# Kernel tuning notes

Measured on AMD Instinct MI355X. Metric: run time of the kernel, lower is better.

## Reference

```python
import jax, jax.numpy as jnp
import numpy as np

DT = 0.2
DX = 0.0327249  # 2*pi/192
KPAD = 2  # (kernel_size-1)//2 for 5x5 periodic 'same' padding
# total derivative order of fd00, fd01, fd10, fd02, fd11, fd20
_ORD = np.array([0, 1, 1, 2, 2, 2], dtype=np.float32)
_SCALES = (DX ** -_ORD)  # FD2d scale = dx^-(jx+jy)


def _poly_apply(w0, b0, w1, b1, wf, bf, x):
    # SymNet (expr.poly): each hidden layer computes two linear combos and
    # appends their product as a new channel; final linear -> scalar.
    o = x @ w0.T + b0                                        # [..., 2]
    x = jnp.concatenate([x, o[..., :1] * o[..., 1:2]], -1)   # [..., 13]
    o = x @ w1.T + b1
    x = jnp.concatenate([x, o[..., :1] * o[..., 1:2]], -1)   # [..., 14]
    return (x @ wf.T + bf)[..., 0]


def _rhs(u, kernels, pw0, pb0, pw1, pb1, pwf, pbf):
    # u: [B, C, H, W]
    B, C, H, W = u.shape
    ks = kernels * jnp.asarray(_SCALES, u.dtype)[:, None, None]   # [6,5,5]
    k01f = -ks[1, :, ::-1]   # -flip along width  (torch flip([3]))
    k10f = -ks[2, ::-1, :]   # -flip along height (torch flip([2]))
    kall = jnp.concatenate([ks, k01f[None], k10f[None]], 0)[:, None]  # [8,1,5,5]
    up = jnp.pad(u, ((0, 0), (0, 0), (KPAD, KPAD), (KPAD, KPAD)), mode='wrap')
    up = up.reshape(B * C, 1, H + 2 * KPAD, W + 2 * KPAD)
    D = jax.lax.conv_general_dilated(up, kall, (1, 1), 'VALID')   # [B*C,8,H,W]
    D = D.reshape(B, C, 8, H, W)
    # per-channel blocks ordered (00,01,10,02,11,20)
    base = jnp.transpose(D[:, :, :6], (0, 3, 4, 1, 2)).reshape(B, H, W, C * 6)
    f01 = jnp.transpose(D[:, :, 6], (0, 2, 3, 1))   # [B,H,W,C]
    f10 = jnp.transpose(D[:, :, 7], (0, 2, 3, 1))
    # upwind: pick normal vs flipped 1st-order stencil by sign of d(poly_k)/d(u01/u10)
    Xsel = base
    for k in range(C):
        pk = (pw0[k], pb0[k], pw1[k], pb1[k], pwf[k], pbf[k])
        G = jax.grad(lambda z: _poly_apply(*pk, z).sum())(base)   # [B,H,W,C*6]
        g01, g10 = G[..., k * 6 + 1], G[..., k * 6 + 2]
        u01 = jnp.where(g01 > 0, base[..., k * 6 + 1], f01[..., k])
        u10 = jnp.where(g10 > 0, base[..., k * 6 + 2], f10[..., k])
        Xsel = Xsel.at[..., k * 6 + 1].set(u01).at[..., k * 6 + 2].set(u10)
    uadd = jnp.stack(
        [_poly_apply(pw0[k], pb0[k], pw1[k], pb1[k], pwf[k], pbf[k], Xsel)
         for k in range(C)], axis=1)                              # [B,C,H,W]
    return uadd


def setup_inputs() -> dict:
    key = jax.random.key(0)
    ks = jax.random.split(key, 8)
    f32 = jnp.float32
    inp = {
        'init': jax.random.normal(ks[0], (16, 2, 192, 192), f32),
        'kernels': jax.random.normal(ks[1], (6, 5, 5), f32) * 0.002,
        'poly_w0': jax.random.normal(ks[2], (2, 2, 12), f32) * 0.01,
        'poly_b0': jax.random.normal(ks[3], (2, 2), f32) * 0.01,
        'poly_w1': jax.random.normal(ks[4], (2, 2, 13), f32) * 0.01,
        'poly_b1': jax.random.normal(ks[5], (2, 2), f32) * 0.01,
        'poly_wf': jax.random.normal(ks[6], (2, 1, 14), f32) * 0.01,
        'poly_bf': jax.random.normal(ks[7], (2, 1), f32) * 0.01,
        'T': 1,
    }
    return inp


def reference(init, kernels, poly_w0, poly_b0, poly_w1, poly_b1, poly_wf, poly_bf, T):
    stepnum = int(round(T / DT))  # 5 RK2 (midpoint) steps
    u = init
    for _ in range(stepnum):
        uh = u + (DT / 2) * _rhs(u, kernels, poly_w0, poly_b0, poly_w1, poly_b1, poly_wf, poly_bf)
        u = u + DT * _rhs(uh, kernels, poly_w0, poly_b0, poly_w1, poly_b1, poly_wf, poly_bf)
    return u
```

## Files before the change

### kernel.cpp

```cpp
#include <hip/hip_runtime.h>

typedef float v2f __attribute__((ext_vector_type(2)));

#define HH 192
#define WW 192
#define BATCH 16
#define PLANE (HH*WW)
#define NELEM (BATCH*2*PLANE)

#define TILEX 96
#define TILEY 8
#define SW 100
#define SH2 12
#define NSITE (SH2*SW)

__global__ void prep_kernel(const float* __restrict__ kern,
                            const float* __restrict__ pw0, const float* __restrict__ pb0,
                            const float* __restrict__ pw1, const float* __restrict__ pb1,
                            const float* __restrict__ pwf, const float* __restrict__ pbf,
                            float* __restrict__ ws)
{
    int t = blockIdx.x * blockDim.x + threadIdx.x;
    if (t < 200) {
        const float inv  = 1.0f / 0.0327249f;
        const float inv2 = inv * inv;
        const float sc[6] = {1.0f, inv, inv, inv2, inv2, inv2};
        int o = t / 8, j = t % 8, dy = o / 5, dx = o % 5;
        float v;
        if (j < 6)       v =  kern[j*25 + dy*5 + dx] * sc[j];
        else if (j == 6) v = -kern[1*25 + dy*5 + (4-dx)] * sc[1];
        else             v = -kern[2*25 + (4-dy)*5 + dx] * sc[2];
        ws[o*8 + j] = v;
    } else if (t < 279) {
        int p = t - 200;
        int arr, a, b;
        if (p < 12)       { arr=0; a=p;      b=24+p; }
        else if (p < 24)  { int i=p-12; arr=0; a=12+i; b=36+i; }
        else if (p == 24) { arr=1; a=0; b=2; }
        else if (p == 25) { arr=1; a=1; b=3; }
        else if (p < 38)  { int i=p-26; arr=2; a=i;    b=26+i; }
        else if (p < 50)  { int i=p-38; arr=2; a=13+i; b=39+i; }
        else if (p == 50) { arr=2; a=12; b=38; }
        else if (p == 51) { arr=2; a=25; b=51; }
        else if (p == 52) { arr=3; a=0; b=2; }
        else if (p == 53) { arr=3; a=1; b=3; }
        else if (p < 68)  { int i=p-54; arr=4; a=i; b=14+i; }
        else if (p == 68) { arr=5; a=0; b=1; }
        else {
            const signed char   A0[10] = {1,2,13,14,1,2,14,15,1,2};
            const signed char   A1[10] = {31,32,43,44,33,34,46,47,21,22};
            const unsigned char AR[10] = {0,0,0,0,2,2,2,2,4,4};
            int i = p - 69; arr = AR[i]; a = A0[i]; b = A1[i];
        }
        const float* bases[6] = {pw0, pb0, pw1, pb1, pwf, pbf};
        v2f v; v[0] = bases[arr][a]; v[1] = bases[arr][b];
        ((v2f*)(ws + 256))[p] = v;
    }
}

__global__ __launch_bounds__(256, 3) void rhs_kernel(
    const float* __restrict__ uin,
    const float* __restrict__ ubase,
    float* __restrict__ uout,
    const float* __restrict__ ws,
    float alpha)
{
    const float* K8T = ws;
    const v2f* PP = (const v2f*)(ws + 256);

    __shared__ v2f sh[SH2][SW];
    const int b   = blockIdx.z;
    const int ty0 = blockIdx.y * TILEY;
    const int tx0 = blockIdx.x * TILEX;
    const int tid = threadIdx.x;
    const size_t bo = (size_t)b * 2 * PLANE;

    const float* uin_b = uin + bo;
    for (int i = tid; i < NSITE; i += 256) {
        const int ly  = i / SW;
        const int col = i - ly * SW;
        int gy = ty0 + ly - 2;  if (gy < 0) gy += HH; else if (gy >= HH) gy -= HH;
        int gx = tx0 + col - 2; if (gx < 0) gx += WW; else if (gx >= WW) gx -= WW;
        const int gi = gy*WW + gx;
        v2f v; v[0] = uin_b[gi]; v[1] = uin_b[PLANE + gi];
        sh[ly][col] = v;
    }
    __syncthreads();

    const int cy = tid >> 5;
    const int x3 = (tid & 31) * 3;

    v2f D2[3][8];
    #pragma unroll
    for (int p = 0; p < 3; ++p)
        #pragma unroll
        for (int j = 0; j < 8; ++j)
            D2[p][j] = (v2f){0.0f, 0.0f};

    #pragma unroll 1
    for (int dy = 0; dy < 5; ++dy) {
        v2f row[7];
        #pragma unroll
        for (int dx = 0; dx < 7; ++dx)
            row[dx] = sh[cy + dy][x3 + dx];
        const float* Kt = K8T + dy * 40;
        #pragma unroll
        for (int dx = 0; dx < 5; ++dx) {
            #pragma unroll
            for (int j = 0; j < 8; ++j) {
                const float w = Kt[dx*8 + j];
                D2[0][j] += row[dx]   * w;
                D2[1][j] += row[dx+1] * w;
                D2[2][j] += row[dx+2] * w;
            }
        }
    }

#define Z(p,i) (D2[p][(i)%6][(i)/6])

    v2f res[3];
    #pragma unroll
    for (int p = 0; p < 3; ++p) {
        v2f o0 = PP[24], o1 = PP[25];
        #pragma unroll
        for (int i = 0; i < 12; ++i) {
            const float zv = Z(p, i);
            o0 += PP[i]    * zv;
            o1 += PP[12+i] * zv;
        }
        const v2f pb = o0 * o1;
        v2f q0 = PP[52] + PP[50]*pb;
        v2f q1 = PP[53] + PP[51]*pb;
        #pragma unroll
        for (int i = 0; i < 12; ++i) {
            const float zv = Z(p, i);
            q0 += PP[26+i] * zv;
            q1 += PP[38+i] * zv;
        }

        const v2f t1 = o1*PP[69] + o0*PP[71];
        const v2f g1 = PP[77] + PP[66]*t1
            + PP[67]*(q1*(PP[73] + PP[50]*t1) + q0*(PP[75] + PP[51]*t1));
        const v2f t2 = o1*PP[70] + o0*PP[72];
        const v2f g2 = PP[78] + PP[66]*t2
            + PP[67]*(q1*(PP[74] + PP[50]*t2) + q0*(PP[76] + PP[51]*t2));

        const float s1 = (g1[0] > 0.0f) ? Z(p,1) : D2[p][6][0];
        const float s2 = (g2[0] > 0.0f) ? Z(p,2) : D2[p][7][0];
        const float s3 = (g1[1] > 0.0f) ? Z(p,7) : D2[p][6][1];
        const float s4 = (g2[1] > 0.0f) ? Z(p,8) : D2[p][7][1];
#define XV(i) ((i)==1 ? s1 : (i)==2 ? s2 : (i)==7 ? s3 : (i)==8 ? s4 : Z(p,(i)))

        v2f f0 = PP[24], f1 = PP[25];
        #pragma unroll
        for (int i = 0; i < 12; ++i) {
            const float xv = XV(i);
            f0 += PP[i]    * xv;
            f1 += PP[12+i] * xv;
        }
        const v2f pf = f0 * f1;
        v2f r0 = PP[52] + PP[50]*pf;
        v2f r1 = PP[53] + PP[51]*pf;
        v2f y  = PP[68] + PP[66]*pf;
        #pragma unroll
        for (int i = 0; i < 12; ++i) {
            const float xv = XV(i);
            r0 += PP[26+i] * xv;
            r1 += PP[38+i] * xv;
            y  += PP[54+i] * xv;
        }
        res[p] = y + PP[67]*(r0*r1);
#undef XV
    }

    const int oy = ty0 + cy, ox = tx0 + x3;
    const size_t o0i = bo + (size_t)oy * WW + ox;
    #pragma unroll
    for (int p = 0; p < 3; ++p) {
        uout[o0i + p]         = ubase[o0i + p]         + alpha * res[p][0];
        uout[o0i + PLANE + p] = ubase[o0i + PLANE + p] + alpha * res[p][1];
    }
}

extern "C" void kernel_launch(void* const* d_in, const int* in_sizes, int n_in,
                              void* d_out, int out_size, void* d_ws, size_t ws_size,
                              hipStream_t stream)
{
    const float* init = (const float*)d_in[0];
    const float* kern = (const float*)d_in[1];
    const float* pw0  = (const float*)d_in[2];
    const float* pb0  = (const float*)d_in[3];
    const float* pw1  = (const float*)d_in[4];
    const float* pb1  = (const float*)d_in[5];
    const float* pwf  = (const float*)d_in[6];
    const float* pbf  = (const float*)d_in[7];
    float* out = (float*)d_out;
    float* ws  = (float*)d_ws;

    float* bufA = ws + 512;
    float* bufH = bufA + NELEM;

    prep_kernel<<<dim3(1), dim3(320), 0, stream>>>(kern, pw0, pb0, pw1, pb1, pwf, pbf, ws);

    const dim3 grid(WW/TILEX, HH/TILEY, BATCH);
    const dim3 block(256);
    const float DTF = 0.2f, DTH = 0.1f;

    rhs_kernel<<<grid, block, 0, stream>>>(init, init, bufH, ws, DTH);
    rhs_kernel<<<grid, block, 0, stream>>>(bufH, init, bufA, ws, DTF);
    for (int s = 0; s < 3; ++s) {
        rhs_kernel<<<grid, block, 0, stream>>>(bufA, bufA, bufH, ws, DTH);
        rhs_kernel<<<grid, block, 0, stream>>>(bufH, bufA, bufA, ws, DTF);
    }
    rhs_kernel<<<grid, block, 0, stream>>>(bufA, bufA, bufH, ws, DTH);
    rhs_kernel<<<grid, block, 0, stream>>>(bufH, bufA, out,  ws, DTF);
}
```

Baseline: 201.3 us.

## Fuse all RK2 stages into one persistent kernel with neighbor-tile flag sync

```diff
diff --git a/kernel.cpp b/kernel.cpp
--- a/kernel.cpp
+++ b/kernel.cpp
@@ -13,6 +13,13 @@
 #define SW 100
 #define SH2 12
 #define NSITE (SH2*SW)
+#define NTILES 768
+#define DTF 0.2f
+#define DTH 0.1f
+
+#define WS_PP    256
+#define WS_FLAGS 512
+#define WS_BUF   8192
 
 __global__ void prep_kernel(const float* __restrict__ kern,
                             const float* __restrict__ pw0, const float* __restrict__ pb0,
@@ -54,131 +61,199 @@
         }
         const float* bases[6] = {pw0, pb0, pw1, pb1, pwf, pbf};
         v2f v; v[0] = bases[arr][a]; v[1] = bases[arr][b];
-        ((v2f*)(ws + 256))[p] = v;
+        ((v2f*)(ws + WS_PP))[p] = v;
     }
+    unsigned* flags = (unsigned*)(ws + WS_FLAGS);
+    for (int i = t; i < 9 * NTILES; i += 320) flags[i] = 0u;
 }
 
-__global__ __launch_bounds__(256, 3) void rhs_kernel(
-    const float* __restrict__ uin,
-    const float* __restrict__ ubase,
-    float* __restrict__ uout,
-    const float* __restrict__ ws,
-    float alpha)
+union DV { double d; v2f v; };
+
+__global__ __launch_bounds__(256, 3) void mega_kernel(
+    const float* __restrict__ init,
+    float* __restrict__ out,
+    float* __restrict__ ws)
 {
     const float* K8T = ws;
-    const v2f* PP = (const v2f*)(ws + 256);
+    const v2f* PP = (const v2f*)(ws + WS_PP);
+    unsigned* flags = (unsigned*)(ws + WS_FLAGS);
+    v2f* P0 = (v2f*)(ws + WS_BUF);
+    v2f* P1 = P0 + (NELEM / 2);
 
     __shared__ v2f sh[SH2][SW];
     const int b   = blockIdx.z;
-    const int ty0 = blockIdx.y * TILEY;
-    const int tx0 = blockIdx.x * TILEX;
+    const int bx  = blockIdx.x;
+    const int by  = blockIdx.y;
+    const int ty0 = by * TILEY;
+    const int tx0 = bx * TILEX;
     const int tid = threadIdx.x;
-    const size_t bo = (size_t)b * 2 * PLANE;
-
-    const float* uin_b = uin + bo;
-    for (int i = tid; i < NSITE; i += 256) {
-        const int ly  = i / SW;
-        const int col = i - ly * SW;
-        int gy = ty0 + ly - 2;  if (gy < 0) gy += HH; else if (gy >= HH) gy -= HH;
-        int gx = tx0 + col - 2; if (gx < 0) gx += WW; else if (gx >= WW) gx -= WW;
-        const int gi = gy*WW + gx;
-        v2f v; v[0] = uin_b[gi]; v[1] = uin_b[PLANE + gi];
-        sh[ly][col] = v;
-    }
-    __syncthreads();
+    const int myflat = b * 48 + by * 2 + bx;
 
     const int cy = tid >> 5;
     const int x3 = (tid & 31) * 3;
-
-    v2f D2[3][8];
-    #pragma unroll
-    for (int p = 0; p < 3; ++p)
+    const int oy = ty0 + cy, ox = tx0 + x3;
+    const size_t site0 = (size_t)b * PLANE + (size_t)oy * WW + ox;
+
+    float base0[3], base1[3];
+
+    #pragma unroll 1
+    for (int s = 0; s < 10; ++s) {
+        const float alpha = (s & 1) ? DTF : DTH;
+        const v2f* Pr = (s & 1) ? P0 : P1;
+        v2f*       Pw = (s & 1) ? P1 : P0;
+
+        if (s) {
+            if (tid < 6) {
+                int ny = by + (tid >> 1) - 1;
+                if (ny < 0) ny += 24; else if (ny >= 24) ny -= 24;
+                const int nc = (tid & 1) ? (1 - bx) : bx;
+                const unsigned* f = flags + (s - 1) * NTILES + (b * 48 + ny * 2 + nc);
+                while (!__hip_atomic_load(f, __ATOMIC_RELAXED, __HIP_MEMORY_SCOPE_AGENT))
+                    __builtin_amdgcn_s_sleep(1);
+            }
+            __syncthreads();
+        }
+
+        if (s == 0) {
+            const float* init_b = init + (size_t)b * 2 * PLANE;
+            for (int i = tid; i < NSITE; i += 256) {
+                const int ly  = i / SW;
+                const int col = i - ly * SW;
+                int gy = ty0 + ly - 2;  if (gy < 0) gy += HH; else if (gy >= HH) gy -= HH;
+                int gx = tx0 + col - 2; if (gx < 0) gx += WW; else if (gx >= WW) gx -= WW;
+                const int gi = gy*WW + gx;
+                v2f v; v[0] = init_b[gi]; v[1] = init_b[PLANE + gi];
+                sh[ly][col] = v;
+            }
+        } else {
+            const v2f* Pb = Pr + (size_t)b * PLANE;
+            for (int i = tid; i < NSITE; i += 256) {
+                const int ly  = i / SW;
+                const int col = i - ly * SW;
+                int gy = ty0 + ly - 2;  if (gy < 0) gy += HH; else if (gy >= HH) gy -= HH;
+                int gx = tx0 + col - 2; if (gx < 0) gx += WW; else if (gx >= WW) gx -= WW;
+                DV cv;
+                cv.d = __hip_atomic_load((const double*)(Pb + gy*WW + gx),
+                                         __ATOMIC_RELAXED, __HIP_MEMORY_SCOPE_AGENT);
+                sh[ly][col] = cv.v;
+            }
+        }
+        __syncthreads();
+
+        if (s == 0) {
+            #pragma unroll
+            for (int p = 0; p < 3; ++p) {
+                const v2f v = sh[cy+2][x3+2+p];
+                base0[p] = v[0]; base1[p] = v[1];
+            }
+        }
+
+        v2f D2[3][8];
         #pragma unroll
-        for (int j = 0; j < 8; ++j)
-            D2[p][j] = (v2f){0.0f, 0.0f};
-
-    #pragma unroll 1
-    for (int dy = 0; dy < 5; ++dy) {
-        v2f row[7];
+        for (int p = 0; p < 3; ++p)
+            #pragma unroll
+            for (int j = 0; j < 8; ++j)
+                D2[p][j] = (v2f){0.0f, 0.0f};
+
+        #pragma unroll 1
+        for (int dy = 0; dy < 5; ++dy) {
+            v2f row[7];
+            #pragma unroll
+            for (int dx = 0; dx < 7; ++dx)
+                row[dx] = sh[cy + dy][x3 + dx];
+            const float* Kt = K8T + dy * 40;
+            #pragma unroll
+            for (int dx = 0; dx < 5; ++dx) {
+                #pragma unroll
+                for (int j = 0; j < 8; ++j) {
+                    const float w = Kt[dx*8 + j];
+                    D2[0][j] += row[dx]   * w;
+                    D2[1][j] += row[dx+1] * w;
+                    D2[2][j] += row[dx+2] * w;
+                }
+            }
+        }
+
+#define Z(p,i) (D2[p][(i)%6][(i)/6])
+
+        v2f res[3];
         #pragma unroll
-        for (int dx = 0; dx < 7; ++dx)
-            row[dx] = sh[cy + dy][x3 + dx];
-        const float* Kt = K8T + dy * 40;
-        #pragma unroll
-        for (int dx = 0; dx < 5; ++dx) {
-            #pragma unroll
-            for (int j = 0; j < 8; ++j) {
-                const float w = Kt[dx*8 + j];
-                D2[0][j] += row[dx]   * w;
-                D2[1][j] += row[dx+1] * w;
-                D2[2][j] += row[dx+2] * w;
-            }
-        }
-    }
-
-#define Z(p,i) (D2[p][(i)%6][(i)/6])
-
-    v2f res[3];
-    #pragma unroll
-    for (int p = 0; p < 3; ++p) {
-        v2f o0 = PP[24], o1 = PP[25];
-        #pragma unroll
-        for (int i = 0; i < 12; ++i) {
-            const float zv = Z(p, i);
-            o0 += PP[i]    * zv;
-            o1 += PP[12+i] * zv;
-        }
-        const v2f pb = o0 * o1;
-        v2f q0 = PP[52] + PP[50]*pb;
-        v2f q1 = PP[53] + PP[51]*pb;
-        #pragma unroll
-        for (int i = 0; i < 12; ++i) {
-            const float zv = Z(p, i);
-            q0 += PP[26+i] * zv;
-            q1 += PP[38+i] * zv;
-        }
-
-        const v2f t1 = o1*PP[69] + o0*PP[71];
-        const v2f g1 = PP[77] + PP[66]*t1
-            + PP[67]*(q1*(PP[73] + PP[50]*t1) + q0*(PP[75] + PP[51]*t1));
-        const v2f t2 = o1*PP[70] + o0*PP[72];
-        const v2f g2 = PP[78] + PP[66]*t2
-            + PP[67]*(q1*(PP[74] + PP[50]*t2) + q0*(PP[76] + PP[51]*t2));
-
-        const float s1 = (g1[0] > 0.0f) ? Z(p,1) : D2[p][6][0];
-        const float s2 = (g2[0] > 0.0f) ? Z(p,2) : D2[p][7][0];
-        const float s3 = (g1[1] > 0.0f) ? Z(p,7) : D2[p][6][1];
-        const float s4 = (g2[1] > 0.0f) ? Z(p,8) : D2[p][7][1];
+        for (int p = 0; p < 3; ++p) {
+            v2f o0 = PP[24], o1 = PP[25];
+            #pragma unroll
+            for (int i = 0; i < 12; ++i) {
+                const float zv = Z(p, i);
+                o0 += PP[i]    * zv;
+                o1 += PP[12+i] * zv;
+            }
+            const v2f pb = o0 * o1;
+            v2f q0 = PP[52] + PP[50]*pb;
+            v2f q1 = PP[53] + PP[51]*pb;
+            #pragma unroll
+            for (int i = 0; i < 12; ++i) {
+                const float zv = Z(p, i);
+                q0 += PP[26+i] * zv;
+                q1 += PP[38+i] * zv;
+            }
+
+            const v2f t1 = o1*PP[69] + o0*PP[71];
+            const v2f g1 = PP[77] + PP[66]*t1
+                + PP[67]*(q1*(PP[73] + PP[50]*t1) + q0*(PP[75] + PP[51]*t1));
+            const v2f t2 = o1*PP[70] + o0*PP[72];
+            const v2f g2 = PP[78] + PP[66]*t2
+                + PP[67]*(q1*(PP[74] + PP[50]*t2) + q0*(PP[76] + PP[51]*t2));
+
+            const float s1 = (g1[0] > 0.0f) ? Z(p,1) : D2[p][6][0];
+            const float s2 = (g2[0] > 0.0f) ? Z(p,2) : D2[p][7][0];
+            const float s3 = (g1[1] > 0.0f) ? Z(p,7) : D2[p][6][1];
+            const float s4 = (g2[1] > 0.0f) ? Z(p,8) : D2[p][7][1];
 #define XV(i) ((i)==1 ? s1 : (i)==2 ? s2 : (i)==7 ? s3 : (i)==8 ? s4 : Z(p,(i)))
 
-        v2f f0 = PP[24], f1 = PP[25];
-        #pragma unroll
-        for (int i = 0; i < 12; ++i) {
-            const float xv = XV(i);
-            f0 += PP[i]    * xv;
-            f1 += PP[12+i] * xv;
-        }
-        const v2f pf = f0 * f1;
-        v2f r0 = PP[52] + PP[50]*pf;
-        v2f r1 = PP[53] + PP[51]*pf;
-        v2f y  = PP[68] + PP[66]*pf;
-        #pragma unroll
-        for (int i = 0; i < 12; ++i) {
-            const float xv = XV(i);
-            r0 += PP[26+i] * xv;
-            r1 += PP[38+i] * xv;
-            y  += PP[54+i] * xv;
-        }
-        res[p] = y + PP[67]*(r0*r1);
+            v2f f0 = PP[24], f1 = PP[25];
+            #pragma unroll
+            for (int i = 0; i < 12; ++i) {
+                const float xv = XV(i);
+                f0 += PP[i]    * xv;
+                f1 += PP[12+i] * xv;
+            }
+            const v2f pf = f0 * f1;
+            v2f r0 = PP[52] + PP[50]*pf;
+            v2f r1 = PP[53] + PP[51]*pf;
+            v2f y  = PP[68] + PP[66]*pf;
+            #pragma unroll
+            for (int i = 0; i < 12; ++i) {
+                const float xv = XV(i);
+                r0 += PP[26+i] * xv;
+                r1 += PP[38+i] * xv;
+                y  += PP[54+i] * xv;
+            }
+            res[p] = y + PP[67]*(r0*r1);
 #undef XV
-    }
-
-    const int oy = ty0 + cy, ox = tx0 + x3;
-    const size_t o0i = bo + (size_t)oy * WW + ox;
-    #pragma unroll
-    for (int p = 0; p < 3; ++p) {
-        uout[o0i + p]         = ubase[o0i + p]         + alpha * res[p][0];
-        uout[o0i + PLANE + p] = ubase[o0i + PLANE + p] + alpha * res[p][1];
+        }
+
+        if (s == 9) {
+            const size_t o0i = (size_t)b * 2 * PLANE + (size_t)oy * WW + ox;
+            #pragma unroll
+            for (int p = 0; p < 3; ++p) {
+                out[o0i + p]         = base0[p] + alpha * res[p][0];
+                out[o0i + PLANE + p] = base1[p] + alpha * res[p][1];
+            }
+        } else {
+            v2f* dst = Pw + site0;
+            #pragma unroll
+            for (int p = 0; p < 3; ++p) {
+                const float w0v = base0[p] + alpha * res[p][0];
+                const float w1v = base1[p] + alpha * res[p][1];
+                DV cv; cv.v = (v2f){w0v, w1v};
+                __hip_atomic_store((double*)(dst + p), cv.d,
+                                   __ATOMIC_RELAXED, __HIP_MEMORY_SCOPE_AGENT);
+                if (s & 1) { base0[p] = w0v; base1[p] = w1v; }
+            }
+            __syncthreads();
+            if (tid == 0)
+                __hip_atomic_store(flags + s * NTILES + myflat, 1u,
+                                   __ATOMIC_RELAXED, __HIP_MEMORY_SCOPE_AGENT);
+        }
     }
 }
 
@@ -197,21 +272,8 @@
     float* out = (float*)d_out;
     float* ws  = (float*)d_ws;
 
-    float* bufA = ws + 512;
-    float* bufH = bufA + NELEM;
-
     prep_kernel<<<dim3(1), dim3(320), 0, stream>>>(kern, pw0, pb0, pw1, pb1, pwf, pbf, ws);
 
     const dim3 grid(WW/TILEX, HH/TILEY, BATCH);
-    const dim3 block(256);
-    const float DTF = 0.2f, DTH = 0.1f;
-
-    rhs_kernel<<<grid, block, 0, stream>>>(init, init, bufH, ws, DTH);
-    rhs_kernel<<<grid, block, 0, stream>>>(bufH, init, bufA, ws, DTF);
-    for (int s = 0; s < 3; ++s) {
-        rhs_kernel<<<grid, block, 0, stream>>>(bufA, bufA, bufH, ws, DTH);
-        rhs_kernel<<<grid, block, 0, stream>>>(bufH, bufA, bufA, ws, DTF);
-    }
-    rhs_kernel<<<grid, block, 0, stream>>>(bufA, bufA, bufH, ws, DTH);
-    rhs_kernel<<<grid, block, 0, stream>>>(bufH, bufA, out,  ws, DTF);
+    mega_kernel<<<grid, dim3(256), 0, stream>>>(init, out, ws);
 }
```

New measurement: 488.8 us. +142.9%, slower.

## Fuse both RK2 midpoint stages into one kernel with halo recomputation

Applied to the files above, without the earlier changes.

```diff
diff --git a/kernel.cpp b/kernel.cpp
--- a/kernel.cpp
+++ b/kernel.cpp
@@ -10,9 +10,14 @@
 
 #define TILEX 96
 #define TILEY 8
-#define SW 100
-#define SH2 12
-#define NSITE (SH2*SW)
+#define SWW 104
+#define SHH 16
+#define UHW 100
+#define UHH 12
+#define NSU (SHH*SWW)
+#define NSH (UHH*UHW)
+#define DTF 0.2f
+#define DTH 0.1f
 
 __global__ void prep_kernel(const float* __restrict__ kern,
                             const float* __restrict__ pw0, const float* __restrict__ pb0,
@@ -58,17 +63,71 @@
     }
 }
 
-__global__ __launch_bounds__(256, 3) void rhs_kernel(
+__device__ __forceinline__ v2f poly_site(const v2f* __restrict__ PP, const v2f D2[8])
+{
+#define Z1(i) (D2[(i)%6][(i)/6])
+    v2f o0 = PP[24], o1 = PP[25];
+    #pragma unroll
+    for (int i = 0; i < 12; ++i) {
+        const float zv = Z1(i);
+        o0 += PP[i]    * zv;
+        o1 += PP[12+i] * zv;
+    }
+    const v2f pb = o0 * o1;
+    v2f q0 = PP[52] + PP[50]*pb;
+    v2f q1 = PP[53] + PP[51]*pb;
+    #pragma unroll
+    for (int i = 0; i < 12; ++i) {
+        const float zv = Z1(i);
+        q0 += PP[26+i] * zv;
+        q1 += PP[38+i] * zv;
+    }
+    const v2f t1 = o1*PP[69] + o0*PP[71];
+    const v2f g1 = PP[77] + PP[66]*t1
+        + PP[67]*(q1*(PP[73] + PP[50]*t1) + q0*(PP[75] + PP[51]*t1));
+    const v2f t2 = o1*PP[70] + o0*PP[72];
+    const v2f g2 = PP[78] + PP[66]*t2
+        + PP[67]*(q1*(PP[74] + PP[50]*t2) + q0*(PP[76] + PP[51]*t2));
+
+    const float s1 = (g1[0] > 0.0f) ? Z1(1) : D2[6][0];
+    const float s2 = (g2[0] > 0.0f) ? Z1(2) : D2[7][0];
+    const float s3 = (g1[1] > 0.0f) ? Z1(7) : D2[6][1];
+    const float s4 = (g2[1] > 0.0f) ? Z1(8) : D2[7][1];
+#define XV1(i) ((i)==1 ? s1 : (i)==2 ? s2 : (i)==7 ? s3 : (i)==8 ? s4 : Z1(i))
+
+    v2f f0 = PP[24], f1 = PP[25];
+    #pragma unroll
+    for (int i = 0; i < 12; ++i) {
+        const float xv = XV1(i);
+        f0 += PP[i]    * xv;
+        f1 += PP[12+i] * xv;
+    }
+    const v2f pf = f0 * f1;
+    v2f r0 = PP[52] + PP[50]*pf;
+    v2f r1 = PP[53] + PP[51]*pf;
+    v2f y  = PP[68] + PP[66]*pf;
+    #pragma unroll
+    for (int i = 0; i < 12; ++i) {
+        const float xv = XV1(i);
+        r0 += PP[26+i] * xv;
+        r1 += PP[38+i] * xv;
+        y  += PP[54+i] * xv;
+    }
+    return y + PP[67]*(r0*r1);
+#undef XV1
+#undef Z1
+}
+
+__global__ __launch_bounds__(256, 3) void step_kernel(
     const float* __restrict__ uin,
-    const float* __restrict__ ubase,
     float* __restrict__ uout,
-    const float* __restrict__ ws,
-    float alpha)
+    const float* __restrict__ ws)
 {
     const float* K8T = ws;
     const v2f* PP = (const v2f*)(ws + 256);
 
-    __shared__ v2f sh[SH2][SW];
+    __shared__ v2f shU[SHH][SWW];
+    __shared__ v2f shH[UHH][UHW];
     const int b   = blockIdx.z;
     const int ty0 = blockIdx.y * TILEY;
     const int tx0 = blockIdx.x * TILEX;
@@ -76,109 +135,86 @@
     const size_t bo = (size_t)b * 2 * PLANE;
 
     const float* uin_b = uin + bo;
-    for (int i = tid; i < NSITE; i += 256) {
-        const int ly  = i / SW;
-        const int col = i - ly * SW;
-        int gy = ty0 + ly - 2;  if (gy < 0) gy += HH; else if (gy >= HH) gy -= HH;
-        int gx = tx0 + col - 2; if (gx < 0) gx += WW; else if (gx >= WW) gx -= WW;
+    for (int i = tid; i < NSU; i += 256) {
+        const int ly  = i / SWW;
+        const int col = i - ly * SWW;
+        int gy = ty0 + ly - 4;  if (gy < 0) gy += HH; else if (gy >= HH) gy -= HH;
+        int gx = tx0 + col - 4; if (gx < 0) gx += WW; else if (gx >= WW) gx -= WW;
         const int gi = gy*WW + gx;
         v2f v; v[0] = uin_b[gi]; v[1] = uin_b[PLANE + gi];
-        sh[ly][col] = v;
+        shU[ly][col] = v;
+    }
+    __syncthreads();
+
+    #pragma unroll 1
+    for (int i = tid; i < NSH; i += 256) {
+        const int ly  = i / UHW;
+        const int col = i - ly * UHW;
+
+        v2f D2[8];
+        #pragma unroll
+        for (int j = 0; j < 8; ++j) D2[j] = (v2f){0.0f, 0.0f};
+
+        #pragma unroll 1
+        for (int dy = 0; dy < 5; ++dy) {
+            v2f w0 = shU[ly+dy][col  ];
+            v2f w1 = shU[ly+dy][col+1];
+            v2f w2 = shU[ly+dy][col+2];
+            v2f w3 = shU[ly+dy][col+3];
+            v2f w4 = shU[ly+dy][col+4];
+            const float* Kt = K8T + dy * 40;
+            #pragma unroll
+            for (int j = 0; j < 8; ++j) {
+                D2[j] += w0 * Kt[j];
+                D2[j] += w1 * Kt[8+j];
+                D2[j] += w2 * Kt[16+j];
+                D2[j] += w3 * Kt[24+j];
+                D2[j] += w4 * Kt[32+j];
+            }
+        }
+
+        const v2f res = poly_site(PP, D2);
+        shH[ly][col] = shU[ly+2][col+2] + DTH * res;
     }
     __syncthreads();
 
     const int cy = tid >> 5;
     const int x3 = (tid & 31) * 3;
 
-    v2f D2[3][8];
+    v2f D2a[3][8];
     #pragma unroll
     for (int p = 0; p < 3; ++p)
         #pragma unroll
         for (int j = 0; j < 8; ++j)
-            D2[p][j] = (v2f){0.0f, 0.0f};
+            D2a[p][j] = (v2f){0.0f, 0.0f};
 
     #pragma unroll 1
     for (int dy = 0; dy < 5; ++dy) {
         v2f row[7];
         #pragma unroll
         for (int dx = 0; dx < 7; ++dx)
-            row[dx] = sh[cy + dy][x3 + dx];
+            row[dx] = shH[cy + dy][x3 + dx];
         const float* Kt = K8T + dy * 40;
         #pragma unroll
         for (int dx = 0; dx < 5; ++dx) {
             #pragma unroll
             for (int j = 0; j < 8; ++j) {
                 const float w = Kt[dx*8 + j];
-                D2[0][j] += row[dx]   * w;
-                D2[1][j] += row[dx+1] * w;
-                D2[2][j] += row[dx+2] * w;
+                D2a[0][j] += row[dx]   * w;
+                D2a[1][j] += row[dx+1] * w;
+                D2a[2][j] += row[dx+2] * w;
             }
         }
     }
 
-#define Z(p,i) (D2[p][(i)%6][(i)/6])
-
-    v2f res[3];
-    #pragma unroll
-    for (int p = 0; p < 3; ++p) {
-        v2f o0 = PP[24], o1 = PP[25];
-        #pragma unroll
-        for (int i = 0; i < 12; ++i) {
-            const float zv = Z(p, i);
-            o0 += PP[i]    * zv;
-            o1 += PP[12+i] * zv;
-        }
-        const v2f pb = o0 * o1;
-        v2f q0 = PP[52] + PP[50]*pb;
-        v2f q1 = PP[53] + PP[51]*pb;
-        #pragma unroll
-        for (int i = 0; i < 12; ++i) {
-            const float zv = Z(p, i);
-            q0 += PP[26+i] * zv;
-            q1 += PP[38+i] * zv;
-        }
-
-        const v2f t1 = o1*PP[69] + o0*PP[71];
-        const v2f g1 = PP[77] + PP[66]*t1
-            + PP[67]*(q1*(PP[73] + PP[50]*t1) + q0*(PP[75] + PP[51]*t1));
-        const v2f t2 = o1*PP[70] + o0*PP[72];
-        const v2f g2 = PP[78] + PP[66]*t2
-            + PP[67]*(q1*(PP[74] + PP[50]*t2) + q0*(PP[76] + PP[51]*t2));
-
-        const float s1 = (g1[0] > 0.0f) ? Z(p,1) : D2[p][6][0];
-        const float s2 = (g2[0] > 0.0f) ? Z(p,2) : D2[p][7][0];
-        const float s3 = (g1[1] > 0.0f) ? Z(p,7) : D2[p][6][1];
-        const float s4 = (g2[1] > 0.0f) ? Z(p,8) : D2[p][7][1];
-#define XV(i) ((i)==1 ? s1 : (i)==2 ? s2 : (i)==7 ? s3 : (i)==8 ? s4 : Z(p,(i)))
-
-        v2f f0 = PP[24], f1 = PP[25];
-        #pragma unroll
-        for (int i = 0; i < 12; ++i) {
-            const float xv = XV(i);
-            f0 += PP[i]    * xv;
-            f1 += PP[12+i] * xv;
-        }
-        const v2f pf = f0 * f1;
-        v2f r0 = PP[52] + PP[50]*pf;
-        v2f r1 = PP[53] + PP[51]*pf;
-        v2f y  = PP[68] + PP[66]*pf;
-        #pragma unroll
-        for (int i = 0; i < 12; ++i) {
-            const float xv = XV(i);
-            r0 += PP[26+i] * xv;
-            r1 += PP[38+i] * xv;
-            y  += PP[54+i] * xv;
-        }
-        res[p] = y + PP[67]*(r0*r1);
-#undef XV
-    }
-
     const int oy = ty0 + cy, ox = tx0 + x3;
     const size_t o0i = bo + (size_t)oy * WW + ox;
     #pragma unroll
     for (int p = 0; p < 3; ++p) {
-        uout[o0i + p]         = ubase[o0i + p]         + alpha * res[p][0];
-        uout[o0i + PLANE + p] = ubase[o0i + PLANE + p] + alpha * res[p][1];
+        const v2f res = poly_site(PP, D2a[p]);
+        const v2f ub  = shU[cy+4][x3+4+p];
+        uout[o0i + p]         = ub[0] + DTF * res[0];
+        uout[o0i + PLANE + p] = ub[1] + DTF * res[1];
     }
 }
 
@@ -198,20 +234,16 @@
     float* ws  = (float*)d_ws;
 
     float* bufA = ws + 512;
-    float* bufH = bufA + NELEM;
+    float* bufB = bufA + NELEM;
 
     prep_kernel<<<dim3(1), dim3(320), 0, stream>>>(kern, pw0, pb0, pw1, pb1, pwf, pbf, ws);
 
     const dim3 grid(WW/TILEX, HH/TILEY, BATCH);
     const dim3 block(256);
-    const float DTF = 0.2f, DTH = 0.1f;
-
-    rhs_kernel<<<grid, block, 0, stream>>>(init, init, bufH, ws, DTH);
-    rhs_kernel<<<grid, block, 0, stream>>>(bufH, init, bufA, ws, DTF);
-    for (int s = 0; s < 3; ++s) {
-        rhs_kernel<<<grid, block, 0, stream>>>(bufA, bufA, bufH, ws, DTH);
-        rhs_kernel<<<grid, block, 0, stream>>>(bufH, bufA, bufA, ws, DTF);
-    }
-    rhs_kernel<<<grid, block, 0, stream>>>(bufA, bufA, bufH, ws, DTH);
-    rhs_kernel<<<grid, block, 0, stream>>>(bufH, bufA, out,  ws, DTF);
-}
+
+    step_kernel<<<grid, block, 0, stream>>>(init, bufA, ws);
+    step_kernel<<<grid, block, 0, stream>>>(bufA, bufB, ws);
+    step_kernel<<<grid, block, 0, stream>>>(bufB, bufA, ws);
+    step_kernel<<<grid, block, 0, stream>>>(bufA, bufB, ws);
+    step_kernel<<<grid, block, 0, stream>>>(bufB, out,  ws);
+}
```

Result: slower. 234.1 us (+16.3%).

## Reuse base poly evaluation incrementally, vectorize halo loads, read base from LDS

Applied to the files above, without the earlier changes.

```diff
diff --git a/kernel.cpp b/kernel.cpp
--- a/kernel.cpp
+++ b/kernel.cpp
@@ -12,7 +12,7 @@
 #define TILEY 8
 #define SW 100
 #define SH2 12
-#define NSITE (SH2*SW)
+#define NPAIR 600
 
 __global__ void prep_kernel(const float* __restrict__ kern,
                             const float* __restrict__ pw0, const float* __restrict__ pb0,
@@ -76,14 +76,17 @@
     const size_t bo = (size_t)b * 2 * PLANE;
 
     const float* uin_b = uin + bo;
-    for (int i = tid; i < NSITE; i += 256) {
-        const int ly  = i / SW;
-        const int col = i - ly * SW;
+    for (int i = tid; i < NPAIR; i += 256) {
+        const int ly  = i / 50;
+        const int cp  = i - ly * 50;
+        const int col = cp * 2;
         int gy = ty0 + ly - 2;  if (gy < 0) gy += HH; else if (gy >= HH) gy -= HH;
-        int gx = tx0 + col - 2; if (gx < 0) gx += WW; else if (gx >= WW) gx -= WW;
-        const int gi = gy*WW + gx;
-        v2f v; v[0] = uin_b[gi]; v[1] = uin_b[PLANE + gi];
-        sh[ly][col] = v;
+        int gx0 = tx0 + col - 2; if (gx0 < 0) gx0 += WW; else if (gx0 >= WW) gx0 -= WW;
+        const int gi = gy*WW + gx0;
+        const float2 a = *(const float2*)(uin_b + gi);
+        const float2 c = *(const float2*)(uin_b + PLANE + gi);
+        float4 st; st.x = a.x; st.y = c.x; st.z = a.y; st.w = c.y;
+        *(float4*)&sh[ly][col] = st;
     }
     __syncthreads();
 
@@ -131,11 +134,13 @@
         const v2f pb = o0 * o1;
         v2f q0 = PP[52] + PP[50]*pb;
         v2f q1 = PP[53] + PP[51]*pb;
+        v2f yb = PP[68] + PP[66]*pb;
         #pragma unroll
         for (int i = 0; i < 12; ++i) {
             const float zv = Z(p, i);
             q0 += PP[26+i] * zv;
             q1 += PP[38+i] * zv;
+            yb += PP[54+i] * zv;
         }
 
         const v2f t1 = o1*PP[69] + o0*PP[71];
@@ -145,40 +150,44 @@
         const v2f g2 = PP[78] + PP[66]*t2
             + PP[67]*(q1*(PP[74] + PP[50]*t2) + q0*(PP[76] + PP[51]*t2));
 
-        const float s1 = (g1[0] > 0.0f) ? Z(p,1) : D2[p][6][0];
-        const float s2 = (g2[0] > 0.0f) ? Z(p,2) : D2[p][7][0];
-        const float s3 = (g1[1] > 0.0f) ? Z(p,7) : D2[p][6][1];
-        const float s4 = (g2[1] > 0.0f) ? Z(p,8) : D2[p][7][1];
-#define XV(i) ((i)==1 ? s1 : (i)==2 ? s2 : (i)==7 ? s3 : (i)==8 ? s4 : Z(p,(i)))
-
-        v2f f0 = PP[24], f1 = PP[25];
-        #pragma unroll
-        for (int i = 0; i < 12; ++i) {
-            const float xv = XV(i);
-            f0 += PP[i]    * xv;
-            f1 += PP[12+i] * xv;
-        }
+        const float d1 = (g1[0] > 0.0f) ? 0.0f : (D2[p][6][0] - Z(p,1));
+        const float d2 = (g2[0] > 0.0f) ? 0.0f : (D2[p][7][0] - Z(p,2));
+        const float d3 = (g1[1] > 0.0f) ? 0.0f : (D2[p][6][1] - Z(p,7));
+        const float d4 = (g2[1] > 0.0f) ? 0.0f : (D2[p][7][1] - Z(p,8));
+
+        v2f f0 = o0 + PP[1]*d1;  f0 += PP[2]*d2;  f0 += PP[7]*d3;  f0 += PP[8]*d4;
+        v2f f1 = o1 + PP[13]*d1; f1 += PP[14]*d2; f1 += PP[19]*d3; f1 += PP[20]*d4;
         const v2f pf = f0 * f1;
-        v2f r0 = PP[52] + PP[50]*pf;
-        v2f r1 = PP[53] + PP[51]*pf;
-        v2f y  = PP[68] + PP[66]*pf;
-        #pragma unroll
-        for (int i = 0; i < 12; ++i) {
-            const float xv = XV(i);
-            r0 += PP[26+i] * xv;
-            r1 += PP[38+i] * xv;
-            y  += PP[54+i] * xv;
-        }
+        const v2f dp = pf - pb;
+        v2f r0 = q0 + PP[27]*d1; r0 += PP[28]*d2; r0 += PP[33]*d3; r0 += PP[34]*d4;
+        r0 += PP[50]*dp;
+        v2f r1 = q1 + PP[39]*d1; r1 += PP[40]*d2; r1 += PP[45]*d3; r1 += PP[46]*d4;
+        r1 += PP[51]*dp;
+        v2f y  = yb + PP[55]*d1; y  += PP[56]*d2; y  += PP[61]*d3; y  += PP[62]*d4;
+        y  += PP[66]*dp;
         res[p] = y + PP[67]*(r0*r1);
-#undef XV
     }
 
     const int oy = ty0 + cy, ox = tx0 + x3;
     const size_t o0i = bo + (size_t)oy * WW + ox;
+    float bb0[3], bb1[3];
+    if (ubase == uin) {
+        #pragma unroll
+        for (int p = 0; p < 3; ++p) {
+            const v2f c = sh[cy+2][x3+2+p];
+            bb0[p] = c[0]; bb1[p] = c[1];
+        }
+    } else {
+        #pragma unroll
+        for (int p = 0; p < 3; ++p) {
+            bb0[p] = ubase[o0i + p];
+            bb1[p] = ubase[o0i + PLANE + p];
+        }
+    }
     #pragma unroll
     for (int p = 0; p < 3; ++p) {
-        uout[o0i + p]         = ubase[o0i + p]         + alpha * res[p][0];
-        uout[o0i + PLANE + p] = ubase[o0i + PLANE + p] + alpha * res[p][1];
+        uout[o0i + p]         = bb0[p] + alpha * res[p][0];
+        uout[o0i + PLANE + p] = bb1[p] + alpha * res[p][1];
     }
 }
 
```

Result: no change. 198.1 us (-1.6%).
